# Performance work log

Hardware: AMD Instinct MI355X
Metric: run time of the kernel (lower is better)

## Reference

```python
import jax, jax.numpy as jnp
import numpy as np

N = 131072
D = 1024
L = 128
B = 64  # number of bags / segments
TEMP = 1.0
EPS = 1e-12  # F.normalize eps


def setup_inputs() -> dict:
    key = jax.random.key(0)
    ks = jax.random.split(key, 5)
    feature = jax.random.normal(ks[0], (N, D), dtype=jnp.float32)
    batch = jnp.sort(jax.random.randint(ks[1], (N,), 0, B)).astype(jnp.int64)
    # xavier_normal_ std = sqrt(2 / (fan_in + fan_out))
    Wa = jax.random.normal(ks[2], (L, D), dtype=jnp.float32) * np.sqrt(2.0 / (D + L))
    Wb = jax.random.normal(ks[3], (L, D), dtype=jnp.float32) * np.sqrt(2.0 / (D + L))
    Wc = jax.random.normal(ks[4], (1, L), dtype=jnp.float32) * np.sqrt(2.0 / (L + 1))
    ba = jnp.zeros((L,), dtype=jnp.float32)
    bb = jnp.zeros((L,), dtype=jnp.float32)
    bc = jnp.zeros((1,), dtype=jnp.float32)
    return {"feature": feature, "batch": batch, "Wa": Wa, "ba": ba,
            "Wb": Wb, "bb": bb, "Wc": Wc, "bc": bc}


def reference(feature, batch, Wa, ba, Wb, bb, Wc, bc):
    # F.normalize: L2-normalize each row
    norm = jnp.linalg.norm(feature, axis=1, keepdims=True)
    feature = feature / jnp.maximum(norm, EPS)

    # gated attention score
    a = jax.nn.sigmoid(feature @ Wa.T + ba)            # [N, L]
    b = jnp.tanh(feature @ Wb.T + bb)                  # [N, L]
    score = ((a * b) @ Wc.T + bc) / TEMP               # [N, 1]

    # segment softmax over bags (torch_geometric softmax(score, batch))
    s = score[:, 0]                                    # [N]
    seg_max = jax.ops.segment_max(s, batch, num_segments=B)
    e = jnp.exp(s - seg_max[batch])
    denom = jax.ops.segment_sum(e, batch, num_segments=B)
    score = (e / denom[batch])[:, None]                # [N, 1]

    # scatter-sum pooling (dropout omitted: eval-mode determinism)
    out = jax.ops.segment_sum(score * feature, batch, num_segments=B)  # [B, D]
    return (out, score, feature)
```

## Files before the change

### kernel.cpp

```cpp
#include <hip/hip_runtime.h>
#include <hip/hip_bf16.h>
#include <cstdint>
#include <cstddef>

#define NROWS 131072
#define DDIM  1024
#define LDIM  128
#define BSEG  64
#define FIX2  281474976710656.0

typedef float f32x4 __attribute__((ext_vector_type(4)));
typedef short short8 __attribute__((ext_vector_type(8)));

__device__ inline unsigned short f2bf(float f) {
    union { float f; unsigned u; } x; x.f = f;
    unsigned u = x.u + 0x7fffu + ((x.u >> 16) & 1u);
    return (unsigned short)(u >> 16);
}

__device__ inline int lower_bound_dev(const int* __restrict__ arr, int n, int v) {
    int lo = 0, hi = n;
    while (lo < hi) { int mid = (lo + hi) >> 1; if (arr[mid] < v) lo = mid + 1; else hi = mid; }
    return lo;
}

__global__ void wconv_kernel(const float* __restrict__ Wa, const float* __restrict__ Wb,
                             unsigned short* __restrict__ wpre) {
    int n  = blockIdx.x;
    int kt = threadIdx.x >> 4;
    int q  = threadIdx.x & 15;
    const float* wrow = (n < LDIM) ? (Wa + (size_t)n * DDIM)
                                   : (Wb + (size_t)(n - LDIM) * DDIM);
    float4 v = *(const float4*)(wrow + kt * 64 + q * 4);
    ushort4 h;
    h.x = f2bf(v.x); h.y = f2bf(v.y); h.z = f2bf(v.z); h.w = f2bf(v.w);
    int w, nfi, rA;
    if (n < LDIM) { w = n >> 4; nfi = 0; rA = n & 15; }
    else { int m = n - LDIM; w = m >> 4; nfi = 1; rA = m & 15; }
    int kk    = q >> 3;
    int e     = (q & 7) * 4;
    int kl    = e >> 3;
    int inner = (e & 7) * 2;
    int lane  = kl * 16 + rA;
    int f     = ((kt * 2 + kk) * 8 + w) * 2 + nfi;
    *(ushort4*)((char*)wpre + f * 1024 + lane * 16 + inner) = h;
}

__global__ __launch_bounds__(512, 6)
void gemm_kernel(const float* __restrict__ feat, const unsigned short* __restrict__ wpre,
                 const float* __restrict__ ba, const float* __restrict__ bb,
                 const float* __restrict__ Wc, const float* __restrict__ bc,
                 const int* __restrict__ batch,
                 float* __restrict__ nf_out, float* __restrict__ s_out,
                 unsigned long long* __restrict__ acc64)
{
    __shared__ __align__(16) char smem[35584];
    float* invA_l = (float*)(smem + 32768);
    float* part   = (float*)(smem + 33024);
    float* u_row  = (float*)(smem + 35072);
    int*   seg_l  = (int*)(smem + 35328);

    const int tid  = threadIdx.x;
    const int w    = tid >> 6;
    const int lane = tid & 63;
    const int rblk = blockIdx.x * 64;
    const int sr   = tid >> 3;
    const int sc8  = tid & 7;

    if (tid < 64) seg_l[tid] = batch[rblk + tid];

    const float4* rowp4 = (const float4*)(feat + (size_t)(rblk + sr) * DDIM);

    f32x4 acc[4][2];
    #pragma unroll
    for (int i = 0; i < 4; ++i)
        #pragma unroll
        for (int j = 0; j < 2; ++j)
            acc[i][j] = (f32x4){0.f, 0.f, 0.f, 0.f};

    const int rA  = lane & 15;
    const int kl  = lane >> 4;
    const int swz = (lane & 7) << 4;
    const char* wsrc = (const char*)wpre + w * 2048 + lane * 16;

    float4 av1_0, av1_1, av2_0, av2_1;
    float sq = 0.f;

    #pragma unroll
    for (int j = 0; j < 2; ++j) {
        int cf = sc8 + j * 8;
        float4 v = rowp4[cf];
        sq += v.x * v.x + v.y * v.y + v.z * v.z + v.w * v.w;
        union { ushort4 h; __hip_bfloat162 b2[2]; } cv;
        cv.b2[0] = __float22bfloat162_rn(make_float2(v.x, v.y));
        cv.b2[1] = __float22bfloat162_rn(make_float2(v.z, v.w));
        *(ushort4*)(smem + ((sr * 128 + cf * 8) ^ ((sr & 7) << 4))) = cv.h;
    }
    av1_0 = rowp4[16 + sc8];
    av1_1 = rowp4[16 + sc8 + 8];
    __syncthreads();

    int cur = 0;
    for (int kt = 0; kt < 16; ++kt) {
        short8 wf[4];
        #pragma unroll
        for (int q = 0; q < 4; ++q)
            wf[q] = *(const short8*)(wsrc + (size_t)kt * 32768 + (q >> 1) * 16384 + (q & 1) * 1024);
        if (kt < 14) {
            av2_0 = rowp4[(kt + 2) * 16 + sc8];
            av2_1 = rowp4[(kt + 2) * 16 + sc8 + 8];
        }
        {
            const char* Abuf = smem + cur * 16384;
            #pragma unroll
            for (int kk = 0; kk < 2; ++kk) {
                int koff = (kk * 64 + kl * 16) ^ swz;
                #pragma unroll
                for (int mf = 0; mf < 4; ++mf) {
                    short8 af = *(const short8*)(Abuf + (mf * 16 + rA) * 128 + koff);
                    #pragma unroll
                    for (int nfi = 0; nfi < 2; ++nfi)
                        acc[mf][nfi] = __builtin_amdgcn_mfma_f32_16x16x32_bf16(
                            af, wf[kk * 2 + nfi], acc[mf][nfi], 0, 0, 0);
                }
            }
        }
        if (kt < 15) {
            char* Ab2 = smem + (cur ^ 1) * 16384;
            #pragma unroll
            for (int j = 0; j < 2; ++j) {
                int cf = sc8 + j * 8;
                float4 v = (j == 0) ? av1_0 : av1_1;
                sq += v.x * v.x + v.y * v.y + v.z * v.z + v.w * v.w;
                union { ushort4 h; __hip_bfloat162 b2[2]; } cv;
                cv.b2[0] = __float22bfloat162_rn(make_float2(v.x, v.y));
                cv.b2[1] = __float22bfloat162_rn(make_float2(v.z, v.w));
                *(ushort4*)(Ab2 + ((sr * 128 + cf * 8) ^ ((sr & 7) << 4))) = cv.h;
            }
        }
        __syncthreads();
        cur ^= 1;
        av1_0 = av2_0; av1_1 = av2_1;
    }

    sq += __shfl_xor(sq, 1, 64);
    sq += __shfl_xor(sq, 2, 64);
    sq += __shfl_xor(sq, 4, 64);
    if (sc8 == 0) invA_l[sr] = 1.f / fmaxf(sqrtf(sq), 1e-12f);
    __syncthreads();

    {
        int l0 = w * 16 + rA;
        float ba0 = ba[l0], bb0 = bb[l0], wc0 = Wc[l0];
        float vals[4][4];
        #pragma unroll
        for (int mf = 0; mf < 4; ++mf)
            #pragma unroll
            for (int reg = 0; reg < 4; ++reg) {
                int r = mf * 16 + kl * 4 + reg;
                float ia = invA_l[r];
                float pa0 = acc[mf][0][reg] * ia + ba0;
                float pb0 = acc[mf][1][reg] * ia + bb0;
                float a0 = 1.f / (1.f + __expf(-pa0));
                float b0 = 1.f - 2.f / (1.f + __expf(2.f * pb0));
                vals[mf][reg] = a0 * b0 * wc0;
            }
        #pragma unroll
        for (int mf = 0; mf < 4; ++mf)
            #pragma unroll
            for (int reg = 0; reg < 4; ++reg) {
                float v = vals[mf][reg];
                v += __shfl_xor(v, 1, 64);
                v += __shfl_xor(v, 2, 64);
                v += __shfl_xor(v, 4, 64);
                v += __shfl_xor(v, 8, 64);
                vals[mf][reg] = v;
            }
        if (rA == 0) {
            #pragma unroll
            for (int mf = 0; mf < 4; ++mf)
                #pragma unroll
                for (int reg = 0; reg < 4; ++reg)
                    part[w * 64 + mf * 16 + kl * 4 + reg] = vals[mf][reg];
        }
    }
    __syncthreads();
    if (tid < 64) {
        float s = part[tid] + part[64 + tid] + part[128 + tid] + part[192 + tid]
                + part[256 + tid] + part[320 + tid] + part[384 + tid] + part[448 + tid] + bc[0];
        u_row[tid] = __expf(s);
        __builtin_nontemporal_store(s, &s_out[rblk + tid]);
    }
    __syncthreads();

    {
        const int col = tid & 255;
        const int grp = tid >> 8;
        const float4* __restrict__ fbase = (const float4*)(feat + (size_t)rblk * DDIM);
        f32x4*        __restrict__ nbase = (f32x4*)(nf_out + (size_t)rblk * DDIM);
        float ax = 0.f, ay = 0.f, az = 0.f, aw = 0.f;
        int curseg = seg_l[grp];
        for (int rr = 0; rr < 8; ++rr) {
            int r0 = rr * 8 + grp;
            float4 v0 = fbase[(r0 + 0) * 256 + col];
            float4 v1 = fbase[(r0 + 2) * 256 + col];
            float4 v2 = fbase[(r0 + 4) * 256 + col];
            float4 v3 = fbase[(r0 + 6) * 256 + col];
            #pragma unroll
            for (int j = 0; j < 4; ++j) {
                int r = r0 + j * 2;
                float4 v = (j == 0) ? v0 : (j == 1) ? v1 : (j == 2) ? v2 : v3;
                int sg = seg_l[r];
                if (sg != curseg) {
                    unsigned long long* dst = acc64 + (size_t)curseg * DDIM + col * 4;
                    atomicAdd(&dst[0], (unsigned long long)(long long)((double)ax * FIX2));
                    atomicAdd(&dst[1], (unsigned long long)(long long)((double)ay * FIX2));
                    atomicAdd(&dst[2], (unsigned long long)(long long)((double)az * FIX2));
                    atomicAdd(&dst[3], (unsigned long long)(long long)((double)aw * FIX2));
                    ax = ay = az = aw = 0.f;
                    curseg = sg;
                }
                float ia = invA_l[r];
                float u  = u_row[r];
                v.x *= ia; v.y *= ia; v.z *= ia; v.w *= ia;
                f32x4 vv = {v.x, v.y, v.z, v.w};
                __builtin_nontemporal_store(vv, &nbase[r * 256 + col]);
                ax += u * v.x; ay += u * v.y; az += u * v.z; aw += u * v.w;
            }
        }
        unsigned long long* dst = acc64 + (size_t)curseg * DDIM + col * 4;
        atomicAdd(&dst[0], (unsigned long long)(long long)((double)ax * FIX2));
        atomicAdd(&dst[1], (unsigned long long)(long long)((double)ay * FIX2));
        atomicAdd(&dst[2], (unsigned long long)(long long)((double)az * FIX2));
        atomicAdd(&dst[3], (unsigned long long)(long long)((double)aw * FIX2));
    }
}

__global__ void softmax_kernel(const int* __restrict__ batch, float* __restrict__ score,
                               float* __restrict__ smax, float* __restrict__ ssum) {
    int b = blockIdx.x;
    int tid = threadIdx.x;
    int start = lower_bound_dev(batch, NROWS, b);
    int end   = lower_bound_dev(batch, NROWS, b + 1);
    __shared__ float red[4];
    __shared__ float bm, bd;

    float m = -INFINITY;
    for (int i = start + tid; i < end; i += 256) m = fmaxf(m, score[i]);
    #pragma unroll
    for (int k = 1; k < 64; k <<= 1) m = fmaxf(m, __shfl_xor(m, k, 64));
    if ((tid & 63) == 0) red[tid >> 6] = m;
    __syncthreads();
    if (tid == 0) bm = fmaxf(fmaxf(red[0], red[1]), fmaxf(red[2], red[3]));
    __syncthreads();
    float M = bm;

    float sum = 0.f;
    for (int i = start + tid; i < end; i += 256) sum += __expf(score[i] - M);
    #pragma unroll
    for (int k = 1; k < 64; k <<= 1) sum += __shfl_xor(sum, k, 64);
    if ((tid & 63) == 0) red[tid >> 6] = sum;
    __syncthreads();
    if (tid == 0) { bd = red[0] + red[1] + red[2] + red[3]; smax[b] = bm; ssum[b] = bd; }
    __syncthreads();
    float invD = 1.f / bd;

    for (int i = start + tid; i < end; i += 256)
        score[i] = __expf(score[i] - M) * invD;
}

__global__ void finalize_kernel(const unsigned long long* __restrict__ acc64,
                                const float* __restrict__ smax, const float* __restrict__ ssum,
                                float* __restrict__ out) {
    int i = blockIdx.x * 256 + threadIdx.x;
    int b = i >> 10;
    double denom = exp((double)smax[b]) * (double)ssum[b];
    out[i] = (float)(((double)(long long)acc64[i]) * (1.0 / FIX2) / denom);
}

extern "C" void kernel_launch(void* const* d_in, const int* in_sizes, int n_in,
                              void* d_out, int out_size, void* d_ws, size_t ws_size,
                              hipStream_t stream) {
    const float* feat  = (const float*)d_in[0];
    const int*   batch = (const int*)d_in[1];
    const float* Wa = (const float*)d_in[2];
    const float* ba = (const float*)d_in[3];
    const float* Wb = (const float*)d_in[4];
    const float* bb = (const float*)d_in[5];
    const float* Wc = (const float*)d_in[6];
    const float* bc = (const float*)d_in[7];

    float* out_seg = (float*)d_out;
    float* score   = out_seg + (size_t)BSEG * DDIM;
    float* nf      = score + NROWS;

    unsigned short*     wpre  = (unsigned short*)d_ws;
    unsigned long long* acc64 = (unsigned long long*)((char*)d_ws + 524288);
    float* smax = (float*)d_ws;
    float* ssum = smax + BSEG;

    hipMemsetAsync(acc64, 0, (size_t)BSEG * DDIM * 8, stream);
    wconv_kernel<<<256, 256, 0, stream>>>(Wa, Wb, wpre);
    gemm_kernel<<<NROWS / 64, 512, 0, stream>>>(feat, wpre, ba, bb, Wc, bc, batch,
                                                nf, score, acc64);
    softmax_kernel<<<BSEG, 256, 0, stream>>>(batch, score, smax, ssum);
    finalize_kernel<<<BSEG * DDIM / 256, 256, 0, stream>>>(acc64, smax, ssum, out_seg);
}
```

Measured before the change: 338.1 us.

## Stage four K-tiles per LDS buffer to cut barriers in GEMM loop

```diff
diff --git a/kernel.cpp b/kernel.cpp
--- a/kernel.cpp
+++ b/kernel.cpp
@@ -46,7 +46,7 @@
     *(ushort4*)((char*)wpre + f * 1024 + lane * 16 + inner) = h;
 }
 
-__global__ __launch_bounds__(512, 6)
+__global__ __launch_bounds__(512, 4)
 void gemm_kernel(const float* __restrict__ feat, const unsigned short* __restrict__ wpre,
                  const float* __restrict__ ba, const float* __restrict__ bb,
                  const float* __restrict__ Wc, const float* __restrict__ bc,
@@ -54,11 +54,11 @@
                  float* __restrict__ nf_out, float* __restrict__ s_out,
                  unsigned long long* __restrict__ acc64)
 {
-    __shared__ __align__(16) char smem[35584];
-    float* invA_l = (float*)(smem + 32768);
-    float* part   = (float*)(smem + 33024);
-    float* u_row  = (float*)(smem + 35072);
-    int*   seg_l  = (int*)(smem + 35328);
+    __shared__ __align__(16) char smem[68352];
+    float* invA_l = (float*)(smem + 65536);
+    float* part   = (float*)(smem + 65792);
+    float* u_row  = (float*)(smem + 67840);
+    int*   seg_l  = (int*)(smem + 68096);
 
     const int tid  = threadIdx.x;
     const int w    = tid >> 6;
@@ -83,41 +83,46 @@
     const int swz = (lane & 7) << 4;
     const char* wsrc = (const char*)wpre + w * 2048 + lane * 16;
 
-    float4 av1_0, av1_1, av2_0, av2_1;
+    float4 av[8];
     float sq = 0.f;
 
     #pragma unroll
-    for (int j = 0; j < 2; ++j) {
-        int cf = sc8 + j * 8;
-        float4 v = rowp4[cf];
-        sq += v.x * v.x + v.y * v.y + v.z * v.z + v.w * v.w;
-        union { ushort4 h; __hip_bfloat162 b2[2]; } cv;
-        cv.b2[0] = __float22bfloat162_rn(make_float2(v.x, v.y));
-        cv.b2[1] = __float22bfloat162_rn(make_float2(v.z, v.w));
-        *(ushort4*)(smem + ((sr * 128 + cf * 8) ^ ((sr & 7) << 4))) = cv.h;
-    }
-    av1_0 = rowp4[16 + sc8];
-    av1_1 = rowp4[16 + sc8 + 8];
-    __syncthreads();
-
-    int cur = 0;
-    for (int kt = 0; kt < 16; ++kt) {
-        short8 wf[4];
-        #pragma unroll
-        for (int q = 0; q < 4; ++q)
-            wf[q] = *(const short8*)(wsrc + (size_t)kt * 32768 + (q >> 1) * 16384 + (q & 1) * 1024);
-        if (kt < 14) {
-            av2_0 = rowp4[(kt + 2) * 16 + sc8];
-            av2_1 = rowp4[(kt + 2) * 16 + sc8 + 8];
-        }
-        {
-            const char* Abuf = smem + cur * 16384;
+    for (int t = 0; t < 4; ++t) {
+        #pragma unroll
+        for (int j = 0; j < 2; ++j) {
+            int cf = sc8 + j * 8;
+            float4 v = rowp4[t * 16 + cf];
+            sq += v.x * v.x + v.y * v.y + v.z * v.z + v.w * v.w;
+            union { ushort4 h; __hip_bfloat162 b2[2]; } cv;
+            cv.b2[0] = __float22bfloat162_rn(make_float2(v.x, v.y));
+            cv.b2[1] = __float22bfloat162_rn(make_float2(v.z, v.w));
+            *(ushort4*)(smem + t * 8192 + ((sr * 128 + cf * 8) ^ ((sr & 7) << 4))) = cv.h;
+        }
+    }
+    #pragma unroll
+    for (int t = 0; t < 4; ++t) {
+        av[t * 2 + 0] = rowp4[(4 + t) * 16 + sc8];
+        av[t * 2 + 1] = rowp4[(4 + t) * 16 + sc8 + 8];
+    }
+    __syncthreads();
+
+    #pragma unroll
+    for (int st = 0; st < 4; ++st) {
+        const int cur = st & 1;
+        const char* Abuf = smem + cur * 32768;
+        #pragma unroll
+        for (int kt4 = 0; kt4 < 4; ++kt4) {
+            const int kt = st * 4 + kt4;
+            short8 wf[4];
+            #pragma unroll
+            for (int q = 0; q < 4; ++q)
+                wf[q] = *(const short8*)(wsrc + (size_t)kt * 32768 + (q >> 1) * 16384 + (q & 1) * 1024);
             #pragma unroll
             for (int kk = 0; kk < 2; ++kk) {
                 int koff = (kk * 64 + kl * 16) ^ swz;
                 #pragma unroll
                 for (int mf = 0; mf < 4; ++mf) {
-                    short8 af = *(const short8*)(Abuf + (mf * 16 + rA) * 128 + koff);
+                    short8 af = *(const short8*)(Abuf + kt4 * 8192 + (mf * 16 + rA) * 128 + koff);
                     #pragma unroll
                     for (int nfi = 0; nfi < 2; ++nfi)
                         acc[mf][nfi] = __builtin_amdgcn_mfma_f32_16x16x32_bf16(
@@ -125,22 +130,30 @@
                 }
             }
         }
-        if (kt < 15) {
-            char* Ab2 = smem + (cur ^ 1) * 16384;
-            #pragma unroll
-            for (int j = 0; j < 2; ++j) {
-                int cf = sc8 + j * 8;
-                float4 v = (j == 0) ? av1_0 : av1_1;
-                sq += v.x * v.x + v.y * v.y + v.z * v.z + v.w * v.w;
-                union { ushort4 h; __hip_bfloat162 b2[2]; } cv;
-                cv.b2[0] = __float22bfloat162_rn(make_float2(v.x, v.y));
-                cv.b2[1] = __float22bfloat162_rn(make_float2(v.z, v.w));
-                *(ushort4*)(Ab2 + ((sr * 128 + cf * 8) ^ ((sr & 7) << 4))) = cv.h;
+        if (st < 3) {
+            char* Ab2 = smem + (cur ^ 1) * 32768;
+            #pragma unroll
+            for (int t = 0; t < 4; ++t) {
+                #pragma unroll
+                for (int j = 0; j < 2; ++j) {
+                    int cf = sc8 + j * 8;
+                    float4 v = av[t * 2 + j];
+                    sq += v.x * v.x + v.y * v.y + v.z * v.z + v.w * v.w;
+                    union { ushort4 h; __hip_bfloat162 b2[2]; } cv;
+                    cv.b2[0] = __float22bfloat162_rn(make_float2(v.x, v.y));
+                    cv.b2[1] = __float22bfloat162_rn(make_float2(v.z, v.w));
+                    *(ushort4*)(Ab2 + t * 8192 + ((sr * 128 + cf * 8) ^ ((sr & 7) << 4))) = cv.h;
+                }
+            }
+            if (st < 2) {
+                #pragma unroll
+                for (int t = 0; t < 4; ++t) {
+                    av[t * 2 + 0] = rowp4[((st + 2) * 4 + t) * 16 + sc8];
+                    av[t * 2 + 1] = rowp4[((st + 2) * 4 + t) * 16 + sc8 + 8];
+                }
             }
         }
         __syncthreads();
-        cur ^= 1;
-        av1_0 = av2_0; av1_1 = av2_1;
     }
 
     sq += __shfl_xor(sq, 1, 64);
```

Result: no change. 337.5 us (-0.2%).
